# Optimization experiments

Measured on AMD Instinct MI355X. Metric: run time of the kernel, lower is better.

Reference implementation:

```python
import jax, jax.numpy as jnp
import numpy as np

N_NODES = 10242
BN_EPS = 1e-5


def _conv(x, idx, w, W, b):
    # x: [N, C]; idx: [N*25*3] int; w: [N, 25, 3]; W: [Cout, 25*C]; b: [Cout]
    n = x.shape[0]
    mat = x[idx].reshape(n, 25, 3, -1)                 # gather: [N,25,3,C]
    agg = jnp.einsum('nkte,nkt->nke', mat, w)          # weighted interp sum over 3 verts
    agg = agg.reshape(n, -1)                           # [N, 25*C]
    return agg @ W.T + b


def _bn_relu(x, g, be):
    # BatchNorm1d in training mode: batch (node-axis) stats, biased variance
    mu = jnp.mean(x, axis=0)
    var = jnp.var(x, axis=0)
    return jax.nn.relu((x - mu) * jax.lax.rsqrt(var + BN_EPS) * g + be)


def setup_inputs() -> dict:
    key = jax.random.key(0)
    ks = jax.random.split(key, 16)
    inp = {}
    inp['x'] = jax.random.normal(ks[0], (N_NODES, 3), dtype=jnp.float32)
    inp['neigh_indices'] = jax.random.randint(ks[1], (N_NODES * 25 * 3,), 0, N_NODES, dtype=jnp.int32)
    w = jax.random.uniform(ks[2], (N_NODES, 25, 3), dtype=jnp.float32)
    inp['neigh_weights'] = w / jnp.sum(w, axis=-1, keepdims=True)  # barycentric-like weights
    def lin(k, cout, cin):
        s = 1.0 / np.sqrt(cin)
        return (jax.random.uniform(k, (cout, cin), dtype=jnp.float32, minval=-s, maxval=s),)
    inp['W1'], = lin(ks[3], 64, 25 * 3);   inp['b1'] = jnp.zeros((64,), jnp.float32)
    inp['g1'] = jnp.ones((64,), jnp.float32);  inp['be1'] = jnp.zeros((64,), jnp.float32)
    inp['W2'], = lin(ks[4], 64, 25 * 64);  inp['b2'] = jnp.zeros((64,), jnp.float32)
    inp['g2'] = jnp.ones((64,), jnp.float32);  inp['be2'] = jnp.zeros((64,), jnp.float32)
    inp['W3'], = lin(ks[5], 128, 25 * 64); inp['b3'] = jnp.zeros((128,), jnp.float32)
    inp['g3'] = jnp.ones((128,), jnp.float32); inp['be3'] = jnp.zeros((128,), jnp.float32)
    inp['Wout'], = lin(ks[6], 36, 25 * 128); inp['bout'] = jnp.zeros((36,), jnp.float32)
    return inp


def reference(x, neigh_indices, neigh_weights, W1, b1, g1, be1, W2, b2, g2, be2,
              W3, b3, g3, be3, Wout, bout):
    h = _bn_relu(_conv(x, neigh_indices, neigh_weights, W1, b1), g1, be1)
    h = _bn_relu(_conv(h, neigh_indices, neigh_weights, W2, b2), g2, be2)
    h = _bn_relu(_conv(h, neigh_indices, neigh_weights, W3, b3), g3, be3)
    out = _conv(h, neigh_indices, neigh_weights, Wout, bout)   # [N, num_classes]
    return out
```

## Files before the change

### kernel.cpp

```cpp
#include <hip/hip_runtime.h>

#define NN 10242

typedef short s8v __attribute__((ext_vector_type(8)));
typedef unsigned int u32x2 __attribute__((ext_vector_type(2)));
typedef float f32x4 __attribute__((ext_vector_type(4)));

static __device__ __forceinline__ float bf2f(unsigned short u) {
    unsigned int i = ((unsigned int)u) << 16;
    return __builtin_bit_cast(float, i);
}
static __device__ __forceinline__ float bfu32lo(unsigned int d) {
    return __builtin_bit_cast(float, d << 16);
}
static __device__ __forceinline__ float bfu32hi(unsigned int d) {
    return __builtin_bit_cast(float, d & 0xffff0000u);
}
static __device__ __forceinline__ unsigned short f2bf(float f) {
    unsigned int i = __builtin_bit_cast(unsigned int, f);
    unsigned int lsb = (i >> 16) & 1u;
    i += 0x7fffu + lsb;
    return (unsigned short)(i >> 16);
}
static __device__ __forceinline__ unsigned int cvtpk(float lo, float hi) {
    unsigned int r;
    asm("v_cvt_pk_bf16_f32 %0, %1, %2" : "=v"(r) : "v"(lo), "v"(hi));
    return r;
}
static __device__ __forceinline__ void gl_lds16(const unsigned short* g, unsigned short* l) {
    __builtin_amdgcn_global_load_lds(
        (const __attribute__((address_space(1))) unsigned int*)g,
        (__attribute__((address_space(3))) unsigned int*)l, 16, 0, 0);
}
template<int N> static __device__ __forceinline__ void waitv() {
    asm volatile("s_waitcnt vmcnt(%0)" :: "n"(N) : "memory");
    __builtin_amdgcn_sched_barrier(0);
}
static __device__ __forceinline__ void lgkm0() {
    asm volatile("s_waitcnt lgkmcnt(0)" ::: "memory");
    __builtin_amdgcn_sched_barrier(0);
}
static __device__ __forceinline__ int imin(int a, int b) { return a < b ? a : b; }

__global__ void detect_k(const void* __restrict__ wgt, int* __restrict__ flag) {
    const float* wf = (const float*)wgt;
    const int r = threadIdx.x;
    float s = wf[3 * r] + wf[3 * r + 1] + wf[3 * r + 2];
    bool ok = (s == s) && (fabsf(s - 1.f) < 0.05f);
    unsigned long long m = __ballot(ok);
    if (r == 0) *flag = (__popcll(m) >= 60) ? 1 : 0;
}

struct Seg { const void* src; void* dst; int n; int nsrc; int mode; int K; int cout; int cpad; };
struct Tab { Seg s[16]; };

__global__ __launch_bounds__(256) void canon_k(Tab t, const int* __restrict__ flag) {
    const Seg sg = t.s[blockIdx.y];
    const bool f32src = (*flag != 0);
    for (int i = blockIdx.x * 256 + threadIdx.x; i < sg.n; i += gridDim.x * 256) {
        if (sg.mode == 0) {
            unsigned short v = 0;
            if (i < sg.nsrc)
                v = f32src ? f2bf(((const float*)sg.src)[i])
                           : ((const unsigned short*)sg.src)[i];
            ((unsigned short*)sg.dst)[i] = v;
        } else if (sg.mode == 1) {
            float v = f32src ? ((const float*)sg.src)[i]
                             : bf2f(((const unsigned short*)sg.src)[i]);
            ((float*)sg.dst)[i] = v;
        } else if (sg.mode == 2) {
            const int row = i / 80, col = i - row * 80;
            unsigned short v = 0;
            if (col < 75) {
                const int j = row * 75 + col;
                v = f32src ? f2bf(((const float*)sg.src)[j])
                           : ((const unsigned short*)sg.src)[j];
            }
            ((unsigned short*)sg.dst)[i] = v;
        } else if (sg.mode == 3) {
            const int e = i & 7;
            const int r = i >> 3;
            const int c = r % sg.cpad;
            const int k8 = r / sg.cpad;
            unsigned short v = 0;
            if (c < sg.cout) {
                const int j = c * sg.K + k8 * 8 + e;
                v = f32src ? f2bf(((const float*)sg.src)[j])
                           : ((const unsigned short*)sg.src)[j];
            }
            ((unsigned short*)sg.dst)[i] = v;
        } else {
            const int row = i >> 2, col = i & 3;
            unsigned short v = 0;
            if (col < 3) {
                const int j = row * 3 + col;
                v = f32src ? f2bf(((const float*)sg.src)[j])
                           : ((const unsigned short*)sg.src)[j];
            }
            ((unsigned short*)sg.dst)[i] = v;
        }
    }
}

template<int CIN4, int COUT, int CG, int NB>
__global__ __launch_bounds__(256) void conv1_k(
    const unsigned short* __restrict__ X4,
    const int* __restrict__ idx,
    const float* __restrict__ wgt,
    const unsigned short* __restrict__ W,
    const float* __restrict__ bias,
    float* __restrict__ Of,
    float* __restrict__ part)
{
    constexpr int K = 75;
    constexpr int KPAD = 80;
    __shared__ unsigned short agg[NB][KPAD];
    __shared__ float ls[256], ls2[256];
    const int tid = threadIdx.x;
    const int n0 = blockIdx.x * NB;

    for (int p = tid; p < NB * 25; p += 256) {
        const int r = p / 25;
        const int k = p - r * 25;
        const int n = n0 + r;
        if (n < NN) {
            const int base = n * 75 + k * 3;
            const int i0 = idx[base], i1 = idx[base + 1], i2 = idx[base + 2];
            const float w0 = wgt[base], w1 = wgt[base + 1], w2 = wgt[base + 2];
            const unsigned long long A = *(const unsigned long long*)(X4 + (size_t)i0 * 4);
            const unsigned long long B = *(const unsigned long long*)(X4 + (size_t)i1 * 4);
            const unsigned long long C = *(const unsigned long long*)(X4 + (size_t)i2 * 4);
            #pragma unroll
            for (int e = 0; e < 3; e++) {
                float v = w0 * bf2f((unsigned short)(A >> (16 * e))) +
                          w1 * bf2f((unsigned short)(B >> (16 * e))) +
                          w2 * bf2f((unsigned short)(C >> (16 * e)));
                agg[r][k * 3 + e] = f2bf(v);
            }
        } else {
            #pragma unroll
            for (int e = 0; e < 3; e++) agg[r][k * 3 + e] = 0;
        }
    }
    for (int p = tid; p < NB * (KPAD - K); p += 256) {
        const int r = p / (KPAD - K);
        agg[r][K + p - r * (KPAD - K)] = 0;
    }
    __syncthreads();

    constexpr int RG = 256 / CG;
    constexpr int RPT = NB / RG;
    const int c = tid % CG;
    const int rq = tid / CG;
    float acc[RPT] = {};
    const unsigned short* Wr = W + (size_t)c * KPAD;
    for (int j = 0; j < KPAD; j += 8) {
        s8v wv = *(const s8v*)(Wr + j);
        float wf[8];
        #pragma unroll
        for (int q = 0; q < 8; q++) wf[q] = bf2f((unsigned short)wv[q]);
        #pragma unroll
        for (int rr = 0; rr < RPT; rr++) {
            s8v av = *(const s8v*)(&agg[rq * RPT + rr][j]);
            #pragma unroll
            for (int q = 0; q < 8; q++)
                acc[rr] += wf[q] * bf2f((unsigned short)av[q]);
        }
    }
    const float bb = bias[c];
    float s = 0.f, s2 = 0.f;
    #pragma unroll
    for (int rr = 0; rr < RPT; rr++) {
        const int n = n0 + rq * RPT + rr;
        if (n < NN) {
            const float v = acc[rr] + bb;
            Of[(size_t)n * COUT + c] = v;
            s += v; s2 += v * v;
        }
    }
    ls[tid] = s; ls2[tid] = s2;
    __syncthreads();
    if (tid < COUT) {
        float a = 0.f, a2 = 0.f;
        #pragma unroll
        for (int g2 = 0; g2 < RG; g2++) {
            a  += ls[g2 * CG + tid];
            a2 += ls2[g2 * CG + tid];
        }
        part[(size_t)blockIdx.x * 2 * COUT + tid] = a;
        part[(size_t)blockIdx.x * 2 * COUT + COUT + tid] = a2;
    }
}

template<int COUTP, int COUT>
__global__ __launch_bounds__(256, 3) void convg_k(
    const unsigned short* __restrict__ X,
    const int* __restrict__ idx,
    const float* __restrict__ wgt,
    const unsigned short* __restrict__ Wt,
    const float* __restrict__ bias,
    float* __restrict__ pre,
    float* __restrict__ part)
{
    constexpr int CIN = 64;
    constexpr int NT = 2;
    constexpr int NFRAG = COUTP / 64;
    constexpr int Q = 2;
    constexpr int R = NT * NFRAG;
    __shared__ unsigned short raw[4 * 64 * CIN];
    __shared__ unsigned short agg[2][16][CIN + 8];
    __shared__ unsigned short iL[25 * 64];
    __shared__ float wL[25 * 48];
    const int tid = threadIdx.x;
    const int n0 = blockIdx.x * 16;

    for (int q = tid; q < 16 * 75; q += 256) {
        const int node = q / 75, f = q - node * 75;
        const int k = f / 3, v = f - k * 3;
        const int n = n0 + node;
        const bool ok = n < NN;
        const int g = ok ? (n * 75 + f) : 0;
        iL[k * 64 + node * 4 + v] = ok ? (unsigned short)idx[g] : 0;
        wL[k * 48 + node * 3 + v] = ok ? wgt[g] : 0.f;
    }
    for (int q = tid; q < 25 * 16; q += 256)
        iL[(q / 16) * 64 + (q - (q / 16) * 16) * 4 + 3] = 0;
    __syncthreads();

    const int wv = tid >> 6;
    const int lane = tid & 63;
    const int l15 = lane & 15;
    const int kg = lane >> 4;
    const int colbase = wv * NFRAG * 16;

    auto issue = [&](int sd) {
        const int base = (sd & 3) * (64 * CIN);
        #pragma unroll
        for (int jj = 0; jj < Q; jj++) {
            const int j = wv * Q + jj;
            const int row = j * 8 + (lane >> 3);
            const int p = lane & 7;
            const int ch = p ^ ((row >> 2) & 7);
            const int id = (int)iL[sd * 64 + row];
            gl_lds16(X + (size_t)id * CIN + ch * 8, &raw[base + j * 512]);
        }
    };
    auto loadB = [&](int sp, s8v* dst) {
        #pragma unroll
        for (int t = 0; t < NT; t++)
            #pragma unroll
            for (int j = 0; j < NFRAG; j++)
                dst[t * NFRAG + j] = *(const s8v*)(Wt +
                    ((size_t)(sp * 8 + t * 4 + kg) * COUTP + colbase + j * 16 + l15) * 8);
    };
    auto interp = [&](int s, int par) {
        const int sb = (s & 3) * (64 * CIN);
        const int node = tid >> 4;
        const int e4 = tid & 15;
        const float w0 = wL[s * 48 + node * 3 + 0];
        const float w1 = wL[s * 48 + node * 3 + 1];
        const float w2 = wL[s * 48 + node * 3 + 2];
        const int chunk = (e4 >> 1) ^ (node & 7);
        const int off = chunk * 8 + (e4 & 1) * 4;
        const int rb = sb + node * 4 * CIN + off;
        const u32x2 A = *(const u32x2*)&raw[rb + 0 * CIN];
        const u32x2 B = *(const u32x2*)&raw[rb + 1 * CIN];
        const u32x2 C = *(const u32x2*)&raw[rb + 2 * CIN];
        const float v0 = w0 * bfu32lo(A[0]) + w1 * bfu32lo(B[0]) + w2 * bfu32lo(C[0]);
        const float v1 = w0 * bfu32hi(A[0]) + w1 * bfu32hi(B[0]) + w2 * bfu32hi(C[0]);
        const float v2 = w0 * bfu32lo(A[1]) + w1 * bfu32lo(B[1]) + w2 * bfu32lo(C[1]);
        const float v3 = w0 * bfu32hi(A[1]) + w1 * bfu32hi(B[1]) + w2 * bfu32hi(C[1]);
        u32x2 o;
        o[0] = cvtpk(v0, v1);
        o[1] = cvtpk(v2, v3);
        *(u32x2*)&agg[par][node][e4 * 4] = o;
    };

    f32x4 acc[NFRAG] = {};
    s8v breg[2][2][R];

    issue(0); issue(1);
    loadB(0, breg[0][0]); loadB(1, breg[0][1]);
    issue(2); issue(3);

    #pragma unroll
    for (int g = 0; g < 12; g++) {
        const int s0 = 2 * g, s1 = 2 * g + 1;
        if (g < 11) { loadB(s0 + 2, breg[(g + 1) & 1][0]); loadB(s0 + 3, breg[(g + 1) & 1][1]); }
        else        { loadB(24, breg[(g + 1) & 1][0]); }
        if (g <= 10) waitv<2 * Q + 2 * R>(); else waitv<Q + R>();
        __builtin_amdgcn_s_barrier();
        interp(s0, 0);
        interp(s1, 1);
        lgkm0();
        __builtin_amdgcn_s_barrier();
        if (s0 + 4 < 25) issue(s0 + 4);
        if (s0 + 5 < 25) issue(s0 + 5);
        __builtin_amdgcn_sched_barrier(0);
        #pragma unroll
        for (int t = 0; t < NT; t++) {
            const s8v a0 = *(const s8v*)(&agg[0][l15][t * 32 + kg * 8]);
            #pragma unroll
            for (int j = 0; j < NFRAG; j++)
                acc[j] = __builtin_amdgcn_mfma_f32_16x16x32_bf16(
                    a0, breg[g & 1][0][t * NFRAG + j], acc[j], 0, 0, 0);
        }
        #pragma unroll
        for (int t = 0; t < NT; t++) {
            const s8v a1 = *(const s8v*)(&agg[1][l15][t * 32 + kg * 8]);
            #pragma unroll
            for (int j = 0; j < NFRAG; j++)
                acc[j] = __builtin_amdgcn_mfma_f32_16x16x32_bf16(
                    a1, breg[g & 1][1][t * NFRAG + j], acc[j], 0, 0, 0);
        }
    }
    waitv<0>();
    __builtin_amdgcn_s_barrier();
    interp(24, 0);
    lgkm0();
    __builtin_amdgcn_s_barrier();
    #pragma unroll
    for (int t = 0; t < NT; t++) {
        const s8v a = *(const s8v*)(&agg[0][l15][t * 32 + kg * 8]);
        #pragma unroll
        for (int j = 0; j < NFRAG; j++)
            acc[j] = __builtin_amdgcn_mfma_f32_16x16x32_bf16(
                a, breg[0][0][t * NFRAG + j], acc[j], 0, 0, 0);
    }

    #pragma unroll
    for (int j = 0; j < NFRAG; j++) {
        const int col = colbase + j * 16 + l15;
        float s = 0.f, s2 = 0.f;
        const float bb = bias[col];
        #pragma unroll
        for (int q = 0; q < 4; q++) {
            const int n = n0 + kg * 4 + q;
            if (n < NN) {
                const float v = acc[j][q] + bb;
                pre[(size_t)n * COUT + col] = v;
                s += v; s2 += v * v;
            }
        }
        s  += __shfl_xor(s, 16);  s  += __shfl_xor(s, 32);
        s2 += __shfl_xor(s2, 16); s2 += __shfl_xor(s2, 32);
        if (kg == 0) {
            part[(size_t)blockIdx.x * 2 * COUT + col] = s;
            part[(size_t)blockIdx.x * 2 * COUT + COUT + col] = s2;
        }
    }
}

template<int CIN, int COUTP, int COUT, int RING, bool FINAL>
__global__ __launch_bounds__(256, 3) void convdma2_k(
    const unsigned short* __restrict__ X,
    const int* __restrict__ idx,
    const float* __restrict__ wgt,
    const unsigned short* __restrict__ Wt,
    const float* __restrict__ bias,
    float* __restrict__ pre,
    void* __restrict__ Ob,
    const int* __restrict__ flag,
    float* __restrict__ part)
{
    constexpr int NT = CIN / 32;
    constexpr int NFRAG = COUTP / 64;
    constexpr int INSTS = CIN / 8;
    constexpr int Q = INSTS / 4;
    constexpr int R = NT * NFRAG;
    constexpr int UPNS = (CIN == 64) ? 4 : 5;
    constexpr int UNITS = 16 << UPNS;
    __shared__ unsigned short raw[RING * 64 * CIN];
    __shared__ unsigned short agg[2][16][CIN + 8];
    __shared__ int   iL[25 * 64];
    __shared__ float wL[25 * 48];
    const int tid = threadIdx.x;
    const int n0 = blockIdx.x * 16;

    for (int q = tid; q < 16 * 75; q += 256) {
        const int node = q / 75, f = q - node * 75;
        const int k = f / 3, v = f - k * 3;
        const int n = n0 + node;
        const bool ok = n < NN;
        const int g = ok ? (n * 75 + f) : 0;
        iL[k * 64 + node * 4 + v] = ok ? idx[g] : 0;
        wL[k * 48 + node * 3 + v] = ok ? wgt[g] : 0.f;
    }
    for (int q = tid; q < 25 * 16; q += 256)
        iL[(q / 16) * 64 + (q - (q / 16) * 16) * 4 + 3] = 0;
    __syncthreads();

    const int wv = tid >> 6;
    const int lane = tid & 63;
    const int l15 = lane & 15;
    const int kg = lane >> 4;
    const int colbase = wv * NFRAG * 16;

    auto issue = [&](int sd) {
        const int base = (sd & (RING - 1)) * (64 * CIN);
        #pragma unroll
        for (int jj = 0; jj < Q; jj++) {
            const int j = wv * Q + jj;
            int row, p;
            if constexpr (CIN == 64) { row = j * 8 + (lane >> 3); p = lane & 7; }
            else                     { row = j * 4 + (lane >> 4); p = lane & 15; }
            const int id = iL[sd * 64 + row];
            gl_lds16(X + (size_t)id * CIN + p * 8, &raw[base + j * 512]);
        }
    };
    auto loadB = [&](int sp, s8v* dst) {
        #pragma unroll
        for (int t = 0; t < NT; t++)
            #pragma unroll
            for (int j = 0; j < NFRAG; j++)
                dst[t * NFRAG + j] = *(const s8v*)(Wt +
                    ((size_t)(sp * (CIN / 8) + t * 4 + kg) * COUTP + colbase + j * 16 + l15) * 8);
    };

    f32x4 acc[NFRAG] = {};
    s8v breg[2][R];

    if constexpr (RING == 4) { issue(0); issue(1); loadB(0, breg[0]); issue(2); }
    else                     { issue(0); loadB(0, breg[0]); issue(1); }

    #pragma unroll
    for (int s = 0; s < 25; s++) {
        if (s + 1 < 25) loadB(s + 1, breg[(s + 1) & 1]);
        if constexpr (RING == 4) {
            if (s <= 22)      waitv<2 * Q + 2 * R>();
            else if (s == 23) waitv<Q + 2 * R>();
            else              waitv<R>();
        } else {
            if (s <= 23)      waitv<Q + 2 * R>();
            else              waitv<R>();
        }
        __builtin_amdgcn_s_barrier();
        {
            const int sb = (s & (RING - 1)) * (64 * CIN);
            #pragma unroll
            for (int u = tid; u < UNITS; u += 256) {
                const int node = u >> UPNS;
                const int e4 = u & ((1 << UPNS) - 1);
                const float w0 = wL[s * 48 + node * 3 + 0];
                const float w1 = wL[s * 48 + node * 3 + 1];
                const float w2 = wL[s * 48 + node * 3 + 2];
                const int rb = sb + node * 4 * CIN + e4 * 4;
                const u32x2 A = *(const u32x2*)&raw[rb + 0 * CIN];
                const u32x2 B = *(const u32x2*)&raw[rb + 1 * CIN];
                const u32x2 C = *(const u32x2*)&raw[rb + 2 * CIN];
                const float v0 = w0 * bfu32lo(A[0]) + w1 * bfu32lo(B[0]) + w2 * bfu32lo(C[0]);
                const float v1 = w0 * bfu32hi(A[0]) + w1 * bfu32hi(B[0]) + w2 * bfu32hi(C[0]);
                const float v2 = w0 * bfu32lo(A[1]) + w1 * bfu32lo(B[1]) + w2 * bfu32lo(C[1]);
                const float v3 = w0 * bfu32hi(A[1]) + w1 * bfu32hi(B[1]) + w2 * bfu32hi(C[1]);
                u32x2 o;
                o[0] = cvtpk(v0, v1);
                o[1] = cvtpk(v2, v3);
                *(u32x2*)&agg[s & 1][node][e4 * 4] = o;
            }
        }
        if constexpr (RING == 4) { if (s + 3 < 25) issue(s + 3); }
        lgkm0();
        __builtin_amdgcn_s_barrier();
        if constexpr (RING == 2) {
            if (s + 2 < 25) issue(s + 2);
            __builtin_amdgcn_sched_barrier(0);
        }
        #pragma unroll
        for (int t = 0; t < NT; t++) {
            const s8v a = *(const s8v*)(&agg[s & 1][l15][t * 32 + kg * 8]);
            #pragma unroll
            for (int j = 0; j < NFRAG; j++)
                acc[j] = __builtin_amdgcn_mfma_f32_16x16x32_bf16(
                    a, breg[s & 1][t * NFRAG + j], acc[j], 0, 0, 0);
        }
    }

    bool f32o = false;
    if constexpr (FINAL) f32o = (*flag != 0);
    #pragma unroll
    for (int j = 0; j < NFRAG; j++) {
        const int col = colbase + j * 16 + l15;
        float s = 0.f, s2 = 0.f;
        if (col < COUT) {
            const float bb = bias[col];
            #pragma unroll
            for (int q = 0; q < 4; q++) {
                const int n = n0 + kg * 4 + q;
                if (n < NN) {
                    const float v = acc[j][q] + bb;
                    if constexpr (FINAL) {
                        if (f32o) ((float*)Ob)[(size_t)n * COUT + col] = v;
                        else ((unsigned short*)Ob)[(size_t)n * COUT + col] = f2bf(v);
                    } else {
                        pre[(size_t)n * COUT + col] = v;
                        s += v; s2 += v * v;
                    }
                }
            }
        }
        if constexpr (!FINAL) {
            s  += __shfl_xor(s, 16);  s  += __shfl_xor(s, 32);
            s2 += __shfl_xor(s2, 16); s2 += __shfl_xor(s2, 32);
            if (kg == 0) {
                part[(size_t)blockIdx.x * 2 * COUT + col] = s;
                part[(size_t)blockIdx.x * 2 * COUT + COUT + col] = s2;
            }
        }
    }
}

template<int C, int NBLK>
__global__ __launch_bounds__(1024) void fin_k(
    const float* __restrict__ part,
    const float* __restrict__ gm,
    const float* __restrict__ bt,
    float* __restrict__ scsh)
{
    constexpr int RG = 1024 / C;
    __shared__ float ls[1024], ls2[1024];
    const int c = threadIdx.x % C;
    const int g = threadIdx.x / C;
    float s = 0.f, s2 = 0.f;
    for (int b = g; b < NBLK; b += RG) {
        s  += part[(size_t)b * 2 * C + c];
        s2 += part[(size_t)b * 2 * C + C + c];
    }
    ls[threadIdx.x] = s; ls2[threadIdx.x] = s2;
    __syncthreads();
    if (threadIdx.x < C) {
        float a = 0.f, a2 = 0.f;
        #pragma unroll
        for (int g2 = 0; g2 < RG; g2++) {
            a  += ls[g2 * C + threadIdx.x];
            a2 += ls2[g2 * C + threadIdx.x];
        }
        const float inv = 1.f / (float)NN;
        float mu = a * inv;
        float var = a2 * inv - mu * mu;
        float scale = gm[threadIdx.x] * rsqrtf(var + 1e-5f);
        scsh[threadIdx.x] = scale;
        scsh[C + threadIdx.x] = bt[threadIdx.x] - mu * scale;
    }
}

template<int C>
__global__ __launch_bounds__(256) void bnap_k(
    const float* __restrict__ pre,
    const float* __restrict__ scsh,
    unsigned short* __restrict__ act)
{
    __shared__ float sc[C], sh[C];
    if (threadIdx.x < C) {
        sc[threadIdx.x] = scsh[threadIdx.x];
        sh[threadIdx.x] = scsh[C + threadIdx.x];
    }
    __syncthreads();
    constexpr int TOTAL4 = NN * C / 4;
    const int stride = gridDim.x * 256;
    for (int i = blockIdx.x * 256 + threadIdx.x; i < TOTAL4; i += stride) {
        const f32x4 v = *(const f32x4*)(pre + (size_t)i * 4);
        const int c0 = (i * 4) % C;
        u32x2 o;
        o[0] = cvtpk(fmaxf(v[0] * sc[c0]     + sh[c0],     0.f),
                     fmaxf(v[1] * sc[c0 + 1] + sh[c0 + 1], 0.f));
        o[1] = cvtpk(fmaxf(v[2] * sc[c0 + 2] + sh[c0 + 2], 0.f),
                     fmaxf(v[3] * sc[c0 + 3] + sh[c0 + 3], 0.f));
        *(u32x2*)(act + (size_t)i * 4) = o;
    }
}

extern "C" void kernel_launch(void* const* d_in, const int* in_sizes, int n_in,
                              void* d_out, int out_size, void* d_ws, size_t ws_size,
                              hipStream_t stream) {
    const void* x    = d_in[0];
    const int*  idx  = (const int*)d_in[1];
    const void* wgt  = d_in[2];
    const void* W1   = d_in[3];
    const void* b1   = d_in[4];
    const void* g1   = d_in[5];
    const void* be1  = d_in[6];
    const void* W2   = d_in[7];
    const void* b2   = d_in[8];
    const void* g2   = d_in[9];
    const void* be2  = d_in[10];
    const void* W3   = d_in[11];
    const void* b3   = d_in[12];
    const void* g3   = d_in[13];
    const void* be3  = d_in[14];
    const void* Wout = d_in[15];
    const void* bout = d_in[16];

    char* ws = (char*)d_ws;
    size_t off = 0;
    auto alloc = [&](size_t bytes) {
        off = (off + 255) & ~(size_t)255;
        size_t o = off; off += bytes; return o;
    };
    const size_t o_flag = alloc(4);
    const size_t o_x4   = alloc((size_t)NN * 4 * 2);
    const size_t o_wgtc = alloc((size_t)NN * 75 * 4);
    const size_t o_W1c  = alloc(64 * 80 * 2);
    const size_t o_Wt2  = alloc((size_t)200 * 64 * 8 * 2);
    const size_t o_Wt3  = alloc((size_t)200 * 128 * 8 * 2);
    const size_t o_Wt4  = alloc((size_t)400 * 64 * 8 * 2);
    const size_t o_bias = alloc(1024 * 4);
    const size_t o_pre  = alloc((size_t)NN * 128 * 4);
    const size_t o_actA = alloc((size_t)NN * 128 * 2);
    const size_t o_actB = alloc((size_t)NN * 64 * 2);
    const size_t o_part = alloc((size_t)641 * 2 * 128 * 4);
    const size_t o_scsh = alloc(2 * 128 * 4);
    if (ws_size < off) return;

    int* flag = (int*)(ws + o_flag);
    unsigned short* x4  = (unsigned short*)(ws + o_x4);
    float* wgtc = (float*)(ws + o_wgtc);
    unsigned short* W1c = (unsigned short*)(ws + o_W1c);
    unsigned short* Wt2 = (unsigned short*)(ws + o_Wt2);
    unsigned short* Wt3 = (unsigned short*)(ws + o_Wt3);
    unsigned short* Wt4 = (unsigned short*)(ws + o_Wt4);
    float* biasc = (float*)(ws + o_bias);
    float* pre  = (float*)(ws + o_pre);
    unsigned short* actA = (unsigned short*)(ws + o_actA);
    unsigned short* actB = (unsigned short*)(ws + o_actB);
    float* part = (float*)(ws + o_part);
    float* scsh = (float*)(ws + o_scsh);

    detect_k<<<1, 64, 0, stream>>>(wgt, flag);

    Tab t;
    t.s[0]  = { x,    x4,   NN * 4,         NN * 3,  4, 0, 0, 0 };
    t.s[1]  = { wgt,  wgtc, NN * 75,        NN * 75, 1, 0, 0, 0 };
    t.s[2]  = { W1,   W1c,  64 * 80,        64 * 80, 2, 0, 0, 0 };
    t.s[3]  = { W2,   Wt2,  200 * 64 * 8,   0,       3, 1600, 64, 64 };
    t.s[4]  = { W3,   Wt3,  200 * 128 * 8,  0,       3, 1600, 128, 128 };
    t.s[5]  = { Wout, Wt4,  400 * 64 * 8,   0,       3, 3200, 36, 64 };
    t.s[6]  = { b1,   biasc + 0,   64, 64, 1, 0, 0, 0 };
    t.s[7]  = { g1,   biasc + 64,  64, 64, 1, 0, 0, 0 };
    t.s[8]  = { be1,  biasc + 128, 64, 64, 1, 0, 0, 0 };
    t.s[9]  = { b2,   biasc + 192, 64, 64, 1, 0, 0, 0 };
    t.s[10] = { g2,   biasc + 256, 64, 64, 1, 0, 0, 0 };
    t.s[11] = { be2,  biasc + 320, 64, 64, 1, 0, 0, 0 };
    t.s[12] = { b3,   biasc + 384, 128, 128, 1, 0, 0, 0 };
    t.s[13] = { g3,   biasc + 512, 128, 128, 1, 0, 0, 0 };
    t.s[14] = { be3,  biasc + 640, 128, 128, 1, 0, 0, 0 };
    t.s[15] = { bout, biasc + 768, 36, 36, 1, 0, 0, 0 };
    canon_k<<<dim3(768, 16), 256, 0, stream>>>(t, flag);

    dim3 B(256);
    conv1_k<4, 64, 64, 16><<<641, B, 0, stream>>>(x4, idx, wgtc, W1c, biasc + 0, pre, part);
    fin_k<64, 641><<<1, 1024, 0, stream>>>(part, biasc + 64, biasc + 128, scsh);
    bnap_k<64><<<512, B, 0, stream>>>(pre, scsh, actA);
    convg_k<64, 64><<<641, B, 0, stream>>>(actA, idx, wgtc, Wt2, biasc + 192, pre, part);
    fin_k<64, 641><<<1, 1024, 0, stream>>>(part, biasc + 256, biasc + 320, scsh);
    bnap_k<64><<<512, B, 0, stream>>>(pre, scsh, actB);
    convg_k<128, 128><<<641, B, 0, stream>>>(actB, idx, wgtc, Wt3, biasc + 384, pre, part);
    fin_k<128, 641><<<1, 1024, 0, stream>>>(part, biasc + 512, biasc + 640, scsh);
    bnap_k<128><<<512, B, 0, stream>>>(pre, scsh, actA);
    convdma2_k<128, 64, 36, 2, true><<<641, B, 0, stream>>>(
        actA, idx, wgtc, Wt4, biasc + 768, nullptr, d_out, flag, nullptr);
}
```

Before: 157.8 us.

## Specialize final conv with half-channel stages, 4-deep ring, and swizzled LDS

```diff
diff --git a/kernel.cpp b/kernel.cpp
--- a/kernel.cpp
+++ b/kernel.cpp
@@ -351,28 +351,23 @@
     }
 }
 
-template<int CIN, int COUTP, int COUT, int RING, bool FINAL>
-__global__ __launch_bounds__(256, 3) void convdma2_k(
+__global__ __launch_bounds__(256, 3) void conv4_k(
     const unsigned short* __restrict__ X,
     const int* __restrict__ idx,
     const float* __restrict__ wgt,
     const unsigned short* __restrict__ Wt,
     const float* __restrict__ bias,
-    float* __restrict__ pre,
     void* __restrict__ Ob,
-    const int* __restrict__ flag,
-    float* __restrict__ part)
+    const int* __restrict__ flag)
 {
-    constexpr int NT = CIN / 32;
-    constexpr int NFRAG = COUTP / 64;
-    constexpr int INSTS = CIN / 8;
-    constexpr int Q = INSTS / 4;
-    constexpr int R = NT * NFRAG;
-    constexpr int UPNS = (CIN == 64) ? 4 : 5;
-    constexpr int UNITS = 16 << UPNS;
-    __shared__ unsigned short raw[RING * 64 * CIN];
-    __shared__ unsigned short agg[2][16][CIN + 8];
-    __shared__ int   iL[25 * 64];
+    constexpr int COUTP = 64;
+    constexpr int COUT = 36;
+    constexpr int NT = 2;
+    constexpr int Q = 2;
+    constexpr int R = 2;
+    __shared__ unsigned short raw[4 * 64 * 64];
+    __shared__ unsigned short agg[2][16][72];
+    __shared__ unsigned short iL[25 * 64];
     __shared__ float wL[25 * 48];
     const int tid = threadIdx.x;
     const int n0 = blockIdx.x * 16;
@@ -383,7 +378,7 @@
         const int n = n0 + node;
         const bool ok = n < NN;
         const int g = ok ? (n * 75 + f) : 0;
-        iL[k * 64 + node * 4 + v] = ok ? idx[g] : 0;
+        iL[k * 64 + node * 4 + v] = ok ? (unsigned short)idx[g] : 0;
         wL[k * 48 + node * 3 + v] = ok ? wgt[g] : 0.f;
     }
     for (int q = tid; q < 25 * 16; q += 256)
@@ -394,116 +389,94 @@
     const int lane = tid & 63;
     const int l15 = lane & 15;
     const int kg = lane >> 4;
-    const int colbase = wv * NFRAG * 16;
-
-    auto issue = [&](int sd) {
-        const int base = (sd & (RING - 1)) * (64 * CIN);
+    const int colbase = wv * 16;
+
+    auto issue = [&](int u) {
+        const int base = (u & 3) * (64 * 64);
+        const int s = u >> 1, h = u & 1;
         #pragma unroll
         for (int jj = 0; jj < Q; jj++) {
             const int j = wv * Q + jj;
-            int row, p;
-            if constexpr (CIN == 64) { row = j * 8 + (lane >> 3); p = lane & 7; }
-            else                     { row = j * 4 + (lane >> 4); p = lane & 15; }
-            const int id = iL[sd * 64 + row];
-            gl_lds16(X + (size_t)id * CIN + p * 8, &raw[base + j * 512]);
+            const int row = j * 8 + (lane >> 3);
+            const int p = lane & 7;
+            const int ch = p ^ ((row >> 2) & 7);
+            const int id = (int)iL[s * 64 + row];
+            gl_lds16(X + (size_t)id * 128 + h * 64 + ch * 8, &raw[base + j * 512]);
         }
     };
-    auto loadB = [&](int sp, s8v* dst) {
+    auto loadB = [&](int u, s8v* dst) {
         #pragma unroll
         for (int t = 0; t < NT; t++)
-            #pragma unroll
-            for (int j = 0; j < NFRAG; j++)
-                dst[t * NFRAG + j] = *(const s8v*)(Wt +
-                    ((size_t)(sp * (CIN / 8) + t * 4 + kg) * COUTP + colbase + j * 16 + l15) * 8);
+            dst[t] = *(const s8v*)(Wt +
+                ((size_t)(u * 8 + t * 4 + kg) * COUTP + colbase + l15) * 8);
     };
-
-    f32x4 acc[NFRAG] = {};
-    s8v breg[2][R];
-
-    if constexpr (RING == 4) { issue(0); issue(1); loadB(0, breg[0]); issue(2); }
-    else                     { issue(0); loadB(0, breg[0]); issue(1); }
+    auto interp = [&](int u, int par) {
+        const int sb = (u & 3) * (64 * 64);
+        const int s = u >> 1;
+        const int node = tid >> 4;
+        const int e4 = tid & 15;
+        const float w0 = wL[s * 48 + node * 3 + 0];
+        const float w1 = wL[s * 48 + node * 3 + 1];
+        const float w2 = wL[s * 48 + node * 3 + 2];
+        const int chunk = (e4 >> 1) ^ (node & 7);
+        const int off = chunk * 8 + (e4 & 1) * 4;
+        const int rb = sb + node * 4 * 64 + off;
+        const u32x2 A = *(const u32x2*)&raw[rb + 0 * 64];
+        const u32x2 B = *(const u32x2*)&raw[rb + 1 * 64];
+        const u32x2 C = *(const u32x2*)&raw[rb + 2 * 64];
+        const float v0 = w0 * bfu32lo(A[0]) + w1 * bfu32lo(B[0]) + w2 * bfu32lo(C[0]);
+        const float v1 = w0 * bfu32hi(A[0]) + w1 * bfu32hi(B[0]) + w2 * bfu32hi(C[0]);
+        const float v2 = w0 * bfu32lo(A[1]) + w1 * bfu32lo(B[1]) + w2 * bfu32lo(C[1]);
+        const float v3 = w0 * bfu32hi(A[1]) + w1 * bfu32hi(B[1]) + w2 * bfu32hi(C[1]);
+        u32x2 o;
+        o[0] = cvtpk(v0, v1);
+        o[1] = cvtpk(v2, v3);
+        *(u32x2*)&agg[par][node][e4 * 4] = o;
+    };
+
+    f32x4 acc = {};
+    s8v breg[2][2][R];
+
+    issue(0); issue(1);
+    loadB(0, breg[0][0]); loadB(1, breg[0][1]);
+    issue(2); issue(3);
 
     #pragma unroll
-    for (int s = 0; s < 25; s++) {
-        if (s + 1 < 25) loadB(s + 1, breg[(s + 1) & 1]);
-        if constexpr (RING == 4) {
-            if (s <= 22)      waitv<2 * Q + 2 * R>();
-            else if (s == 23) waitv<Q + 2 * R>();
-            else              waitv<R>();
-        } else {
-            if (s <= 23)      waitv<Q + 2 * R>();
-            else              waitv<R>();
-        }
+    for (int g = 0; g < 25; g++) {
+        const int u0 = 2 * g, u1 = 2 * g + 1;
+        if (g < 24) { loadB(u0 + 2, breg[(g + 1) & 1][0]); loadB(u0 + 3, breg[(g + 1) & 1][1]); }
+        if (g <= 23) waitv<2 * Q + 2 * R>(); else waitv<0>();
         __builtin_amdgcn_s_barrier();
-        {
-            const int sb = (s & (RING - 1)) * (64 * CIN);
-            #pragma unroll
-            for (int u = tid; u < UNITS; u += 256) {
-                const int node = u >> UPNS;
-                const int e4 = u & ((1 << UPNS) - 1);
-                const float w0 = wL[s * 48 + node * 3 + 0];
-                const float w1 = wL[s * 48 + node * 3 + 1];
-                const float w2 = wL[s * 48 + node * 3 + 2];
-                const int rb = sb + node * 4 * CIN + e4 * 4;
-                const u32x2 A = *(const u32x2*)&raw[rb + 0 * CIN];
-                const u32x2 B = *(const u32x2*)&raw[rb + 1 * CIN];
-                const u32x2 C = *(const u32x2*)&raw[rb + 2 * CIN];
-                const float v0 = w0 * bfu32lo(A[0]) + w1 * bfu32lo(B[0]) + w2 * bfu32lo(C[0]);
-                const float v1 = w0 * bfu32hi(A[0]) + w1 * bfu32hi(B[0]) + w2 * bfu32hi(C[0]);
-                const float v2 = w0 * bfu32lo(A[1]) + w1 * bfu32lo(B[1]) + w2 * bfu32lo(C[1]);
-                const float v3 = w0 * bfu32hi(A[1]) + w1 * bfu32hi(B[1]) + w2 * bfu32hi(C[1]);
-                u32x2 o;
-                o[0] = cvtpk(v0, v1);
-                o[1] = cvtpk(v2, v3);
-                *(u32x2*)&agg[s & 1][node][e4 * 4] = o;
-            }
-        }
-        if constexpr (RING == 4) { if (s + 3 < 25) issue(s + 3); }
+        interp(u0, 0);
+        interp(u1, 1);
         lgkm0();
         __builtin_amdgcn_s_barrier();
-        if constexpr (RING == 2) {
-            if (s + 2 < 25) issue(s + 2);
-            __builtin_amdgcn_sched_barrier(0);
-        }
+        if (u0 + 4 < 50) issue(u0 + 4);
+        if (u0 + 5 < 50) issue(u0 + 5);
+        __builtin_amdgcn_sched_barrier(0);
         #pragma unroll
         for (int t = 0; t < NT; t++) {
-            const s8v a = *(const s8v*)(&agg[s & 1][l15][t * 32 + kg * 8]);
-            #pragma unroll
-            for (int j = 0; j < NFRAG; j++)
-                acc[j] = __builtin_amdgcn_mfma_f32_16x16x32_bf16(
-                    a, breg[s & 1][t * NFRAG + j], acc[j], 0, 0, 0);
-        }
-    }
-
-    bool f32o = false;
-    if constexpr (FINAL) f32o = (*flag != 0);
-    #pragma unroll
-    for (int j = 0; j < NFRAG; j++) {
-        const int col = colbase + j * 16 + l15;
-        float s = 0.f, s2 = 0.f;
-        if (col < COUT) {
-            const float bb = bias[col];
-            #pragma unroll
-            for (int q = 0; q < 4; q++) {
-                const int n = n0 + kg * 4 + q;
-                if (n < NN) {
-                    const float v = acc[j][q] + bb;
-                    if constexpr (FINAL) {
-                        if (f32o) ((float*)Ob)[(size_t)n * COUT + col] = v;
-                        else ((unsigned short*)Ob)[(size_t)n * COUT + col] = f2bf(v);
-                    } else {
-                        pre[(size_t)n * COUT + col] = v;
-                        s += v; s2 += v * v;
-                    }
-                }
-            }
-        }
-        if constexpr (!FINAL) {
-            s  += __shfl_xor(s, 16);  s  += __shfl_xor(s, 32);
-            s2 += __shfl_xor(s2, 16); s2 += __shfl_xor(s2, 32);
-            if (kg == 0) {
-                part[(size_t)blockIdx.x * 2 * COUT + col] = s;
-                part[(size_t)blockIdx.x * 2 * COUT + COUT + col] = s2;
+            const s8v a0 = *(const s8v*)(&agg[0][l15][t * 32 + kg * 8]);
+            acc = __builtin_amdgcn_mfma_f32_16x16x32_bf16(a0, breg[g & 1][0][t], acc, 0, 0, 0);
+        }
+        #pragma unroll
+        for (int t = 0; t < NT; t++) {
+            const s8v a1 = *(const s8v*)(&agg[1][l15][t * 32 + kg * 8]);
+            acc = __builtin_amdgcn_mfma_f32_16x16x32_bf16(a1, breg[g & 1][1][t], acc, 0, 0, 0);
+        }
+    }
+
+    const bool f32o = (*flag != 0);
+    const int col = colbase + l15;
+    if (col < COUT) {
+        const float bb = bias[col];
+        #pragma unroll
+        for (int q = 0; q < 4; q++) {
+            const int n = n0 + kg * 4 + q;
+            if (n < NN) {
+                const float v = acc[q] + bb;
+                if (f32o) ((float*)Ob)[(size_t)n * COUT + col] = v;
+                else      ((unsigned short*)Ob)[(size_t)n * COUT + col] = f2bf(v);
             }
         }
     }
@@ -656,6 +629,5 @@
     convg_k<128, 128><<<641, B, 0, stream>>>(actB, idx, wgtc, Wt3, biasc + 384, pre, part);
     fin_k<128, 641><<<1, 1024, 0, stream>>>(part, biasc + 512, biasc + 640, scsh);
     bnap_k<128><<<512, B, 0, stream>>>(pre, scsh, actA);
-    convdma2_k<128, 64, 36, 2, true><<<641, B, 0, stream>>>(
-        actA, idx, wgtc, Wt4, biasc + 768, nullptr, d_out, flag, nullptr);
-}
+    conv4_k<<<641, B, 0, stream>>>(actA, idx, wgtc, Wt4, biasc + 768, d_out, flag);
+}
```

Result: no change. 157.2 us (-0.4%).
